# Kernel tuning notes

Hardware: AMD Instinct MI355X
Metric: run time of the kernel (lower is better)

The kernel has to match this reference:

```python
import jax, jax.numpy as jnp
import numpy as np

B, T, C, H = 8, 1024, 1024, 16
D = C // H
EPS = 1e-5

def _ln(x, g, b):
    mu = jnp.mean(x, axis=-1, keepdims=True)
    var = jnp.var(x, axis=-1, keepdims=True)
    return (x - mu) * jax.lax.rsqrt(var + EPS) * g + b

def _build_mask(cond_mask, cond_len, token_len):
    # Vectorized form of the per-batch Python-loop mask in the torch module.
    counts = jnp.sum(cond_mask, axis=-1)            # [B] number of valid cond tokens
    rows = jnp.arange(T)
    cols = jnp.arange(T)
    # all rows may attend to the first counts[i] (cond) columns
    m_cond = cols[None, None, :] < counts[:, None, None]          # [B,1,T]
    m_cond = jnp.broadcast_to(m_cond, (B, T, T))
    # block-causal tiled pattern on rows/cols >= cond_len:
    # value = (col - cond_len) % token_len <= (row - cond_len) % token_len
    pattern = ((cols[None, :] - cond_len) % token_len) <= ((rows[:, None] - cond_len) % token_len)
    m_block = (rows[:, None] >= cond_len) & (cols[None, :] >= cond_len) & pattern  # [T,T]
    # cols >= cond_len: overwritten by block pattern (rows < cond_len stay 0 there)
    mask = jnp.where(cols[None, None, :] < cond_len, m_cond, m_block[None, :, :])
    return mask[:, None, :, :]                      # [B,1,T,T] bool

def _attn(x, Wq, bq, Wk, bk, Wv, bv, Wp, bp, cond_mask, cond_len, token_len):
    q = (x @ Wq + bq).reshape(B, T, H, D).transpose(0, 2, 1, 3)  # [B,H,T,D]
    k = (x @ Wk + bk).reshape(B, T, H, D).transpose(0, 2, 1, 3)
    v = (x @ Wv + bv).reshape(B, T, H, D).transpose(0, 2, 1, 3)
    att = jnp.einsum('bhqd,bhkd->bhqk', q, k) * (1.0 / np.sqrt(D))
    mask = _build_mask(cond_mask, cond_len, token_len)
    att = jnp.where(mask, att, -jnp.inf)
    att = jax.nn.softmax(att, axis=-1)
    y = jnp.einsum('bhqk,bhkd->bhqd', att, v)
    y = y.transpose(0, 2, 1, 3).reshape(B, T, C)
    return y @ Wp + bp

def setup_inputs() -> dict:
    key = jax.random.key(0)
    ks = jax.random.split(key, 16)
    cond_len, token_len = 256, 768
    s = 1.0 / np.sqrt(C)
    counts = jax.random.randint(ks[0], (B,), 1, cond_len + 1)
    cond_mask = (jnp.arange(T)[None, :] < counts[:, None]).astype(jnp.int32)
    return {
        'x': jax.random.normal(ks[1], (B, T, C), jnp.float32),
        'ln1_g': jnp.ones((C,), jnp.float32), 'ln1_b': jnp.zeros((C,), jnp.float32),
        'Wq': jax.random.normal(ks[2], (C, C), jnp.float32) * s, 'bq': jnp.zeros((C,), jnp.float32),
        'Wk': jax.random.normal(ks[3], (C, C), jnp.float32) * s, 'bk': jnp.zeros((C,), jnp.float32),
        'Wv': jax.random.normal(ks[4], (C, C), jnp.float32) * s, 'bv': jnp.zeros((C,), jnp.float32),
        'Wp': jax.random.normal(ks[5], (C, C), jnp.float32) * s, 'bp': jnp.zeros((C,), jnp.float32),
        'ln2_g': jnp.ones((C,), jnp.float32), 'ln2_b': jnp.zeros((C,), jnp.float32),
        'W1': jax.random.normal(ks[6], (C, 4 * C), jnp.float32) * s, 'b1': jnp.zeros((4 * C,), jnp.float32),
        'W2': jax.random.normal(ks[7], (4 * C, C), jnp.float32) * (0.5 * s), 'b2': jnp.zeros((C,), jnp.float32),
        'cond_mask': cond_mask,
        'cond_len': cond_len,
        'token_len': token_len,
    }

def reference(x, ln1_g, ln1_b, Wq, bq, Wk, bk, Wv, bv, Wp, bp, ln2_g, ln2_b, W1, b1, W2, b2, cond_mask, cond_len, token_len):
    x = x + _attn(_ln(x, ln1_g, ln1_b), Wq, bq, Wk, bk, Wv, bv, Wp, bp, cond_mask, cond_len, token_len)
    h = _ln(x, ln2_g, ln2_b)
    x = x + (jax.nn.gelu(h @ W1 + b1, approximate=False) @ W2 + b2)
    return x
```

## Files before the change

kernel.cpp:

```cpp
#include <hip/hip_runtime.h>
#include <hip/hip_bf16.h>
#include <cstdint>
#include <cstddef>

typedef __attribute__((ext_vector_type(8))) short short8;
typedef __attribute__((ext_vector_type(4))) float f32x4;
typedef __attribute__((ext_vector_type(4))) unsigned short us4;

#define MFMA_BF16(a, b, c) __builtin_amdgcn_mfma_f32_16x16x32_bf16((a), (b), (c), 0, 0, 0)
#define VMCNT(n) asm volatile("s_waitcnt vmcnt(" #n ")" ::: "memory")

__device__ __forceinline__ unsigned short f2bf(float f) {
  unsigned int u = __float_as_uint(f);
  u += 0x7FFFu + ((u >> 16) & 1u);
  return (unsigned short)(u >> 16);
}

typedef const void __attribute__((address_space(1)))* as1_cvp;
typedef void __attribute__((address_space(3)))* as3_vp;
__device__ __forceinline__ void gll16(const short* g, short* l) {
#if defined(__HIP_DEVICE_COMPILE__)
  __builtin_amdgcn_global_load_lds((as1_cvp)g, (as3_vp)l, 16, 0, 0);
#else
  (void)g; (void)l;
#endif
}

__global__ void count_kernel(const int* __restrict__ cm, int* __restrict__ counts) {
  __shared__ int sd[256];
  const int b = blockIdx.x, t = threadIdx.x;
  int s = 0;
  for (int i = t; i < 1024; i += 256) s += cm[b * 1024 + i];
  sd[t] = s; __syncthreads();
  for (int k = 128; k > 0; k >>= 1) { if (t < k) sd[t] += sd[t + k]; __syncthreads(); }
  if (t == 0) counts[b] = sd[0];
}

__global__ void pack_bias_kernel(const float* __restrict__ bq, const float* __restrict__ bk,
                                 const float* __restrict__ bv, float* __restrict__ dst) {
  int i = blockIdx.x * 256 + threadIdx.x;
  dst[i] = (i < 1024) ? bq[i] : (i < 2048 ? bk[i - 1024] : bv[i - 2048]);
}

__global__ void transpose_kernel(const float* __restrict__ src, unsigned short* __restrict__ dst,
                                 int R, int C) {
  __shared__ float tile[32][33];
  const int c0 = blockIdx.x * 32, r0 = blockIdx.y * 32;
  const int tx = threadIdx.x, ty = threadIdx.y;
  #pragma unroll
  for (int i = ty; i < 32; i += 8)
    tile[i][tx] = src[(size_t)(r0 + i) * C + (c0 + tx)];
  __syncthreads();
  #pragma unroll
  for (int i = ty; i < 32; i += 8)
    dst[(size_t)(c0 + i) * R + (r0 + tx)] = f2bf(tile[tx][i]);
}

__global__ void vtrans_kernel(const short* __restrict__ qkv, short* __restrict__ vtr) {
  __shared__ short tile[32][33];
  const int bh = blockIdx.z;
  const int t0 = blockIdx.x * 32, d0 = blockIdx.y * 32;
  const int b = bh >> 4, h = bh & 15;
  const int tx = threadIdx.x, ty = threadIdx.y;
  const short* src = qkv + (size_t)b * 1024 * 3072 + 2048 + h * 64;
  #pragma unroll
  for (int i = ty; i < 32; i += 8)
    tile[i][tx] = src[(size_t)(t0 + i) * 3072 + d0 + tx];
  __syncthreads();
  short* dst = vtr + (size_t)bh * 65536;
  #pragma unroll
  for (int i = ty; i < 32; i += 8)
    dst[(d0 + i) * 1024 + t0 + tx] = tile[tx][i];
}

__global__ __launch_bounds__(256) void ln_kernel(const float* __restrict__ in,
                                                 const float* __restrict__ gw,
                                                 const float* __restrict__ bw,
                                                 unsigned short* __restrict__ out) {
  const int row = blockIdx.x, t = threadIdx.x;
  const float4 v = ((const float4*)(in + (size_t)row * 1024))[t];
  float s = v.x + v.y + v.z + v.w;
  float ss = v.x * v.x + v.y * v.y + v.z * v.z + v.w * v.w;
  #pragma unroll
  for (int o = 32; o >= 1; o >>= 1) { s += __shfl_down(s, o, 64); ss += __shfl_down(ss, o, 64); }
  __shared__ float red[8];
  if ((t & 63) == 0) { red[t >> 6] = s; red[4 + (t >> 6)] = ss; }
  __syncthreads();
  const float S  = red[0] + red[1] + red[2] + red[3];
  const float SS = red[4] + red[5] + red[6] + red[7];
  const float mu = S * (1.0f / 1024.0f);
  const float var = SS * (1.0f / 1024.0f) - mu * mu;
  const float rs = rsqrtf(var + 1e-5f);
  const int c = t * 4;
  const float4 g4 = ((const float4*)gw)[t];
  const float4 b4 = ((const float4*)bw)[t];
  us4 o4;
  o4[0] = f2bf((v.x - mu) * rs * g4.x + b4.x);
  o4[1] = f2bf((v.y - mu) * rs * g4.y + b4.y);
  o4[2] = f2bf((v.z - mu) * rs * g4.z + b4.z);
  o4[3] = f2bf((v.w - mu) * rs * g4.w + b4.w);
  *(us4*)(out + (size_t)row * 1024 + c) = o4;
}

template <int EPI>
__global__ __launch_bounds__(512, 1) void gemm_k2_kernel(
    const short* __restrict__ A, const short* __restrict__ BT,
    const float* __restrict__ bias, int N, int K, int gm,
    unsigned short* __restrict__ outb, float* __restrict__ outf,
    const float* __restrict__ res) {
  __shared__ alignas(16) short lds[73728];
  const int t = threadIdx.x;
  const int l = t & 63, w = t >> 6;
  const int lq = l & 15, g = l >> 4;
  const int wr = w >> 2, wc = w & 3;
  const int cpx = (int)gridDim.x >> 3;
  const int wid = ((int)blockIdx.x & 7) * cpx + ((int)blockIdx.x >> 3);
  const int bm = (wid % gm) * 256, bn = (wid / gm) * 128;
  const int NT = K >> 6;

  const int csw = ((t & 7) ^ ((t >> 3) & 7)) * 8;
  const int sA = t >> 3;
  const int sB = ((t >> 8) & 1) * 64 + ((t >> 3) & 31);

  const f32x4 z4 = {0.f, 0.f, 0.f, 0.f};
  f32x4 acc[8][2];
  #pragma unroll
  for (int i = 0; i < 8; i++) { acc[i][0] = z4; acc[i][1] = z4; }

  auto stageA = [&](int buf, int h, int k0) {
    const short* src = A + (size_t)(bm + h * 64 + sA) * K + k0 + csw;
    short* dst = lds + buf * 24576 + h * 8192 + t * 8;
    gll16(src, dst);
    gll16(src + (size_t)128 * K, dst + 4096);
  };
  auto stageB = [&](int buf, int h, int k0) {
    const short* src = BT + (size_t)(bn + h * 32 + sB) * K + k0 + csw;
    short* dst = lds + buf * 24576 + 16384 + h * 4096 + t * 8;
    gll16(src, dst);
  };
  auto rdA = [&](int buf, int mh, int mi2, int kk) {
    const int ra = wr * 64 + mi2 * 16 + lq;
    const int unit = (kk * 4 + g) ^ (ra & 7);
    return *(const short8*)(lds + buf * 24576 + mh * 8192 + ra * 64 + unit * 8);
  };
  auto rdB = [&](int buf, int ni2, int kk) {
    const int h = wc & 1;
    const int rb = (wc >> 1) * 32 + ni2 * 16 + lq;
    const int unit = (kk * 4 + g) ^ (rb & 7);
    return *(const short8*)(lds + buf * 24576 + 16384 + h * 4096 + rb * 64 + unit * 8);
  };

  stageA(0, 0, 0);  stageB(0, 0, 0);
  stageA(0, 1, 0);  stageB(0, 1, 0);
  stageA(1, 0, 64); stageB(1, 0, 64);
  VMCNT(3);
  __builtin_amdgcn_s_barrier();

  int cur = 0;
  for (int v = 0; v < NT; ++v) {
    const int nx1 = (cur == 2) ? 0 : cur + 1;
    const int nx2 = (nx1 == 2) ? 0 : nx1 + 1;
    short8 a[4][2], b[2][2], a2[4][2];
    #pragma unroll
    for (int mi2 = 0; mi2 < 4; ++mi2)
      #pragma unroll
      for (int kk = 0; kk < 2; ++kk) a[mi2][kk] = rdA(cur, 0, mi2, kk);
    #pragma unroll
    for (int ni2 = 0; ni2 < 2; ++ni2)
      #pragma unroll
      for (int kk = 0; kk < 2; ++kk) b[ni2][kk] = rdB(cur, ni2, kk);
    if (v + 1 < NT) { stageA(nx1, 1, (v + 1) * 64); stageB(nx1, 1, (v + 1) * 64); }
    __builtin_amdgcn_s_setprio(1);
    #pragma unroll
    for (int mi2 = 0; mi2 < 4; ++mi2)
      #pragma unroll
      for (int ni2 = 0; ni2 < 2; ++ni2)
        #pragma unroll
        for (int kk = 0; kk < 2; ++kk)
          acc[mi2][ni2] = MFMA_BF16(a[mi2][kk], b[ni2][kk], acc[mi2][ni2]);
    __builtin_amdgcn_s_setprio(0);
    #pragma unroll
    for (int mi2 = 0; mi2 < 4; ++mi2)
      #pragma unroll
      for (int kk = 0; kk < 2; ++kk) a2[mi2][kk] = rdA(cur, 1, mi2, kk);
    if (v + 2 < NT) {
      stageA(nx2, 0, (v + 2) * 64); stageB(nx2, 0, (v + 2) * 64);
      VMCNT(3);
    } else {
      VMCNT(0);
    }
    __builtin_amdgcn_s_barrier();
    __builtin_amdgcn_s_setprio(1);
    #pragma unroll
    for (int mi2 = 0; mi2 < 4; ++mi2)
      #pragma unroll
      for (int ni2 = 0; ni2 < 2; ++ni2)
        #pragma unroll
        for (int kk = 0; kk < 2; ++kk)
          acc[4 + mi2][ni2] = MFMA_BF16(a2[mi2][kk], b[ni2][kk], acc[4 + mi2][ni2]);
    __builtin_amdgcn_s_setprio(0);
    cur = nx1;
  }

  if (EPI == 2) {
    #pragma unroll
    for (int mi = 0; mi < 8; ++mi) {
      #pragma unroll
      for (int ni = 0; ni < 2; ++ni) {
        const int col = bn + wc * 32 + ni * 16 + lq;
        const float bv = bias[col];
        #pragma unroll
        for (int r = 0; r < 4; ++r) {
          const int row = bm + wr * 128 + (mi >> 2) * 64 + (mi & 3) * 16 + 4 * g + r;
          const size_t idx = (size_t)row * N + col;
          outf[idx] = acc[mi][ni][r] + bv + res[idx];
        }
      }
    }
    return;
  }

  unsigned short* eb = (unsigned short*)lds;
  #pragma unroll
  for (int mi = 0; mi < 8; ++mi) {
    #pragma unroll
    for (int ni = 0; ni < 2; ++ni) {
      const int col = wc * 32 + ni * 16 + lq;
      const float bv = bias[bn + col];
      #pragma unroll
      for (int r = 0; r < 4; ++r) {
        const int row = wr * 128 + (mi >> 2) * 64 + (mi & 3) * 16 + 4 * g + r;
        float vv = acc[mi][ni][r] + bv;
        if (EPI == 1) vv = 0.5f * vv * (1.0f + erff(vv * 0.70710678118654752440f));
        eb[row * 128 + col] = f2bf(vv);
      }
    }
  }
  __syncthreads();
  #pragma unroll
  for (int it = 0; it < 8; ++it) {
    const int unit = it * 512 + t;
    const int row = unit >> 4, c8 = unit & 15;
    const short8 vv = *(const short8*)(lds + unit * 8);
    *(short8*)((short*)outb + (size_t)(bm + row) * N + bn + c8 * 8) = vv;
  }
}

__global__ __launch_bounds__(64) void attn_kernel(
    const short* __restrict__ qkv, const short* __restrict__ vtr,
    unsigned short* __restrict__ y, const int* __restrict__ counts) {
  const int blk = blockIdx.x;
  const int slot = blk >> 3;
  const int p = slot & 31;
  const int bh = ((slot >> 5) << 3) | (blk & 7);
  const int b = bh >> 4, h = bh & 15;
  const int l = threadIdx.x & 63;
  const int lq = l & 15, g = l >> 4;
  const int qb0 = p * 16, qb1 = (63 - p) * 16;
  const int count = counts[b];

  const short* base  = qkv + (size_t)b * 1024 * 3072 + h * 64;
  const short* vbase = vtr + (size_t)bh * 65536;

  short8 qf[2][2];
  {
    const short* qr0 = base + (size_t)(qb0 + lq) * 3072 + 8 * g;
    const short* qr1 = base + (size_t)(qb1 + lq) * 3072 + 8 * g;
    qf[0][0] = *(const short8*)qr0; qf[0][1] = *(const short8*)(qr0 + 32);
    qf[1][0] = *(const short8*)qr1; qf[1][1] = *(const short8*)(qr1 + 32);
  }

  const f32x4 z4 = {0.f, 0.f, 0.f, 0.f};
  f32x4 oacc[2][4];
  #pragma unroll
  for (int grp = 0; grp < 2; ++grp)
    #pragma unroll
    for (int dc = 0; dc < 4; ++dc) oacc[grp][dc] = z4;
  float mrun[2] = {-1e30f, -1e30f};
  float lrun[2] = {0.f, 0.f};
  const int permrow = 8 * (lq >> 2) + (lq & 3);
  const float SC = 0.125f * 1.44269504088896f;

  const int ncond = min((count + 31) >> 5, 8);
  const int ncausal = (qb1 + 16 - 256 + 31) >> 5;
  const int nt = ncond + ncausal;
  auto kv_of = [&](int i) { return i < ncond ? i * 32 : 256 + (i - ncond) * 32; };

  auto loadt = [&](int kv0, short8 (&kr)[4], short8 (&vr)[4]) {
    const short* ka = base + (size_t)(kv0 + permrow) * 3072 + 1024 + 8 * g;
    kr[0] = *(const short8*)ka;
    kr[1] = *(const short8*)(ka + 32);
    kr[2] = *(const short8*)(ka + 4 * 3072);
    kr[3] = *(const short8*)(ka + 4 * 3072 + 32);
    #pragma unroll
    for (int dc = 0; dc < 4; ++dc)
      vr[dc] = *(const short8*)(vbase + (16 * dc + lq) * 1024 + kv0 + 8 * g);
  };

  auto compute = [&](int i, const short8 (&kr)[4], const short8 (&vr)[4]) {
    const int kv0 = kv_of(i);
    const bool isCond = (i < ncond);
    #pragma unroll
    for (int grp = 0; grp < 2; ++grp) {
      const int qb = grp ? qb1 : qb0;
      if (!isCond && kv0 >= qb + 16) continue;
      const bool needMask = isCond ? (kv0 + 32 > count) : (kv0 + 31 > qb);
      f32x4 sA = z4, sB = z4;
      __builtin_amdgcn_s_setprio(1);
      sA = MFMA_BF16(kr[0], qf[grp][0], sA);
      sA = MFMA_BF16(kr[1], qf[grp][1], sA);
      sB = MFMA_BF16(kr[2], qf[grp][0], sB);
      sB = MFMA_BF16(kr[3], qf[grp][1], sB);
      __builtin_amdgcn_s_setprio(0);
      const int q = qb + lq;
      float mx = -1e30f;
      if (needMask) {
        #pragma unroll
        for (int r = 0; r < 4; ++r) {
          const int colA = kv0 + 8 * g + r, colB = colA + 4;
          const bool okA = isCond ? (colA < count) : (colA <= q);
          const bool okB = isCond ? (colB < count) : (colB <= q);
          const float vA = okA ? sA[r] * SC : -1e30f;
          const float vB = okB ? sB[r] * SC : -1e30f;
          sA[r] = vA; sB[r] = vB;
          mx = fmaxf(fmaxf(vA, vB), mx);
        }
      } else {
        #pragma unroll
        for (int r = 0; r < 4; ++r) {
          const float vA = sA[r] * SC, vB = sB[r] * SC;
          sA[r] = vA; sB[r] = vB;
          mx = fmaxf(fmaxf(vA, vB), mx);
        }
      }
      mx = fmaxf(mx, __shfl_xor(mx, 16, 64));
      mx = fmaxf(mx, __shfl_xor(mx, 32, 64));
      float m = mrun[grp];
      if (!__all(mx <= m + 8.0f)) {
        const float mn = fmaxf(m, mx);
        const float sf = exp2f(m - mn);
        lrun[grp] *= sf;
        #pragma unroll
        for (int dc = 0; dc < 4; ++dc)
          #pragma unroll
          for (int r = 0; r < 4; ++r) oacc[grp][dc][r] *= sf;
        mrun[grp] = mn; m = mn;
      }
      float ps = 0.f;
      #pragma unroll
      for (int r = 0; r < 4; ++r) {
        const float aa = exp2f(sA[r] - m);
        const float c2 = exp2f(sB[r] - m);
        sA[r] = aa; sB[r] = c2; ps += aa + c2;
      }
      ps += __shfl_xor(ps, 16, 64);
      ps += __shfl_xor(ps, 32, 64);
      lrun[grp] += ps;
      union { short8 s8; __hip_bfloat162 h2[4]; } pu;
      pu.h2[0] = __float22bfloat162_rn(float2{sA[0], sA[1]});
      pu.h2[1] = __float22bfloat162_rn(float2{sA[2], sA[3]});
      pu.h2[2] = __float22bfloat162_rn(float2{sB[0], sB[1]});
      pu.h2[3] = __float22bfloat162_rn(float2{sB[2], sB[3]});
      __builtin_amdgcn_s_setprio(1);
      #pragma unroll
      for (int dc = 0; dc < 4; ++dc)
        oacc[grp][dc] = MFMA_BF16(vr[dc], pu.s8, oacc[grp][dc]);
      __builtin_amdgcn_s_setprio(0);
    }
  };

  short8 kb0[4], vb0[4], kb1[4], vb1[4];
  loadt(kv_of(0), kb0, vb0);
  for (int i = 0; i < nt; i += 2) {
    if (i + 1 < nt) loadt(kv_of(i + 1), kb1, vb1);
    compute(i, kb0, vb0);
    if (i + 1 >= nt) break;
    if (i + 2 < nt) loadt(kv_of(i + 2), kb0, vb0);
    compute(i + 1, kb1, vb1);
  }

  #pragma unroll
  for (int grp = 0; grp < 2; ++grp) {
    const int qb = grp ? qb1 : qb0;
    const float inv = 1.0f / lrun[grp];
    unsigned short* yr = y + (size_t)(b * 1024 + qb + lq) * 1024 + h * 64;
    #pragma unroll
    for (int dc = 0; dc < 4; ++dc)
      #pragma unroll
      for (int r = 0; r < 4; ++r)
        yr[16 * dc + 4 * g + r] = f2bf(oacc[grp][dc][r] * inv);
  }
}

extern "C" void kernel_launch(void* const* d_in, const int* in_sizes, int n_in,
                              void* d_out, int out_size, void* d_ws, size_t ws_size,
                              hipStream_t stream) {
  (void)in_sizes; (void)n_in; (void)out_size; (void)ws_size;
  const float* x     = (const float*)d_in[0];
  const float* ln1_g = (const float*)d_in[1];
  const float* ln1_b = (const float*)d_in[2];
  const float* Wq    = (const float*)d_in[3];
  const float* bq    = (const float*)d_in[4];
  const float* Wk    = (const float*)d_in[5];
  const float* bk    = (const float*)d_in[6];
  const float* Wv    = (const float*)d_in[7];
  const float* bv    = (const float*)d_in[8];
  const float* Wp    = (const float*)d_in[9];
  const float* bp    = (const float*)d_in[10];
  const float* ln2_g = (const float*)d_in[11];
  const float* ln2_b = (const float*)d_in[12];
  const float* W1    = (const float*)d_in[13];
  const float* b1    = (const float*)d_in[14];
  const float* W2    = (const float*)d_in[15];
  const float* b2    = (const float*)d_in[16];
  const int* cond_mask = (const int*)d_in[17];

  char* ws = (char*)d_ws;
  const size_t MB = 1u << 20;
  short* xn    = (short*)(ws + 0);
  short* vtr   = (short*)(ws + 0);
  short* qkv   = (short*)(ws + 16 * MB);
  short* act   = (short*)(ws + 0);
  unsigned short* yb = (unsigned short*)(ws + 64 * MB);
  float* x1    = (float*)(ws + 80 * MB);
  short* hb    = (short*)(ws + 112 * MB);
  short* wqkvT = (short*)(ws + 128 * MB);
  short* wpT   = (short*)(ws + 134 * MB);
  short* w1T   = (short*)(ws + 136 * MB);
  short* w2T   = (short*)(ws + 144 * MB);
  float* bqkv  = (float*)(ws + 152 * MB);
  int* counts  = (int*)(ws + 152 * MB + 16384);

  const dim3 tb(32, 8);
  count_kernel<<<8, 256, 0, stream>>>(cond_mask, counts);
  pack_bias_kernel<<<12, 256, 0, stream>>>(bq, bk, bv, bqkv);
  transpose_kernel<<<dim3(32, 32), tb, 0, stream>>>(Wq, (unsigned short*)wqkvT, 1024, 1024);
  transpose_kernel<<<dim3(32, 32), tb, 0, stream>>>(Wk, (unsigned short*)(wqkvT + 1024 * 1024), 1024, 1024);
  transpose_kernel<<<dim3(32, 32), tb, 0, stream>>>(Wv, (unsigned short*)(wqkvT + 2 * 1024 * 1024), 1024, 1024);
  transpose_kernel<<<dim3(32, 32), tb, 0, stream>>>(Wp, (unsigned short*)wpT, 1024, 1024);
  transpose_kernel<<<dim3(128, 32), tb, 0, stream>>>(W1, (unsigned short*)w1T, 1024, 4096);
  transpose_kernel<<<dim3(32, 128), tb, 0, stream>>>(W2, (unsigned short*)w2T, 4096, 1024);
  ln_kernel<<<8192, 256, 0, stream>>>(x, ln1_g, ln1_b, (unsigned short*)xn);

  gemm_k2_kernel<0><<<768, 512, 0, stream>>>(xn, wqkvT, bqkv, 3072, 1024, 32,
                                             (unsigned short*)qkv, nullptr, nullptr);
  vtrans_kernel<<<dim3(32, 2, 128), tb, 0, stream>>>(qkv, vtr);
  attn_kernel<<<4096, 64, 0, stream>>>(qkv, vtr, yb, counts);
  gemm_k2_kernel<2><<<256, 512, 0, stream>>>((const short*)yb, wpT, bp, 1024, 1024, 32,
                                             nullptr, x1, x);
  ln_kernel<<<8192, 256, 0, stream>>>(x1, ln2_g, ln2_b, (unsigned short*)hb);
  gemm_k2_kernel<1><<<1024, 512, 0, stream>>>(hb, w1T, b1, 4096, 1024, 32,
                                              (unsigned short*)act, nullptr, nullptr);
  gemm_k2_kernel<2><<<256, 512, 0, stream>>>(act, w2T, b2, 1024, 4096, 32,
                                             nullptr, (float*)d_out, x1);
}
```

Baseline: 471.5 us.

## Add 128x256 GEMM tile kernel for QKV and MLP-up projections

```diff
diff --git a/kernel.cpp b/kernel.cpp
--- a/kernel.cpp
+++ b/kernel.cpp
@@ -103,11 +103,137 @@
 }
 
 template <int EPI>
+__global__ __launch_bounds__(512, 1) void gemm_n256_kernel(
+    const short* __restrict__ A, const short* __restrict__ BT,
+    const float* __restrict__ bias, int N, int K, int gm,
+    unsigned short* __restrict__ outb) {
+  __shared__ alignas(16) short lds[73728];
+  const int t = threadIdx.x;
+  const int l = t & 63, w = t >> 6;
+  const int lq = l & 15, g = l >> 4;
+  const int wr = w >> 2, wc = w & 3;
+  const int cpx = (int)gridDim.x >> 3;
+  const int wid = ((int)blockIdx.x & 7) * cpx + ((int)blockIdx.x >> 3);
+  const int bm = (wid % gm) * 128, bn = (wid / gm) * 256;
+  const int NT = K >> 6;
+
+  const int csw = ((t & 7) ^ ((t >> 3) & 7)) * 8;
+  const int sr = t >> 3;
+
+  const f32x4 z4 = {0.f, 0.f, 0.f, 0.f};
+  f32x4 acc[4][4];
+  #pragma unroll
+  for (int i = 0; i < 4; i++)
+    #pragma unroll
+    for (int j = 0; j < 4; j++) acc[i][j] = z4;
+
+  auto stageA = [&](int buf, int k0) {
+    const short* src = A + (size_t)(bm + sr) * K + k0 + csw;
+    short* dst = lds + buf * 24576 + t * 8;
+    gll16(src, dst);
+    gll16(src + (size_t)64 * K, dst + 4096);
+  };
+  auto stageB = [&](int buf, int h, int k0) {
+    const short* src = BT + (size_t)(bn + h * 128 + sr) * K + k0 + csw;
+    short* dst = lds + buf * 24576 + 8192 + h * 8192 + t * 8;
+    gll16(src, dst);
+    gll16(src + (size_t)64 * K, dst + 4096);
+  };
+  auto rdA = [&](int buf, int mi2, int kk) {
+    const int ra = wr * 64 + mi2 * 16 + lq;
+    const int unit = (kk * 4 + g) ^ (ra & 7);
+    return *(const short8*)(lds + buf * 24576 + ra * 64 + unit * 8);
+  };
+  auto rdB = [&](int buf, int h, int ni2, int kk) {
+    const int cb = wc * 32 + ni2 * 16 + lq;
+    const int unit = (kk * 4 + g) ^ (cb & 7);
+    return *(const short8*)(lds + buf * 24576 + 8192 + h * 8192 + cb * 64 + unit * 8);
+  };
+
+  stageA(0, 0);     stageB(0, 0, 0);
+  stageB(0, 1, 0);
+  stageA(1, 64);    stageB(1, 0, 64);
+  VMCNT(4);
+  __builtin_amdgcn_s_barrier();
+
+  int cur = 0;
+  for (int v = 0; v < NT; ++v) {
+    const int nx1 = (cur == 2) ? 0 : cur + 1;
+    const int nx2 = (nx1 == 2) ? 0 : nx1 + 1;
+    short8 a[4][2], b[2][2], b2[2][2];
+    #pragma unroll
+    for (int mi2 = 0; mi2 < 4; ++mi2)
+      #pragma unroll
+      for (int kk = 0; kk < 2; ++kk) a[mi2][kk] = rdA(cur, mi2, kk);
+    #pragma unroll
+    for (int ni2 = 0; ni2 < 2; ++ni2)
+      #pragma unroll
+      for (int kk = 0; kk < 2; ++kk) b[ni2][kk] = rdB(cur, 0, ni2, kk);
+    if (v + 1 < NT) stageB(nx1, 1, (v + 1) * 64);
+    __builtin_amdgcn_s_setprio(1);
+    #pragma unroll
+    for (int mi2 = 0; mi2 < 4; ++mi2)
+      #pragma unroll
+      for (int ni2 = 0; ni2 < 2; ++ni2)
+        #pragma unroll
+        for (int kk = 0; kk < 2; ++kk)
+          acc[mi2][ni2] = MFMA_BF16(a[mi2][kk], b[ni2][kk], acc[mi2][ni2]);
+    __builtin_amdgcn_s_setprio(0);
+    #pragma unroll
+    for (int ni2 = 0; ni2 < 2; ++ni2)
+      #pragma unroll
+      for (int kk = 0; kk < 2; ++kk) b2[ni2][kk] = rdB(cur, 1, ni2, kk);
+    if (v + 2 < NT) {
+      stageA(nx2, (v + 2) * 64); stageB(nx2, 0, (v + 2) * 64);
+      VMCNT(4);
+    } else {
+      VMCNT(0);
+    }
+    __builtin_amdgcn_s_barrier();
+    __builtin_amdgcn_s_setprio(1);
+    #pragma unroll
+    for (int mi2 = 0; mi2 < 4; ++mi2)
+      #pragma unroll
+      for (int ni2 = 0; ni2 < 2; ++ni2)
+        #pragma unroll
+        for (int kk = 0; kk < 2; ++kk)
+          acc[mi2][2 + ni2] = MFMA_BF16(a[mi2][kk], b2[ni2][kk], acc[mi2][2 + ni2]);
+    __builtin_amdgcn_s_setprio(0);
+    cur = nx1;
+  }
+
+  __syncthreads();
+  unsigned short* eb = (unsigned short*)lds;
+  #pragma unroll
+  for (int mi2 = 0; mi2 < 4; ++mi2) {
+    #pragma unroll
+    for (int n = 0; n < 4; ++n) {
+      const int col = (n >> 1) * 128 + wc * 32 + (n & 1) * 16 + lq;
+      const float bv = bias[bn + col];
+      #pragma unroll
+      for (int r = 0; r < 4; ++r) {
+        const int row = wr * 64 + mi2 * 16 + 4 * g + r;
+        float vv = acc[mi2][n][r] + bv;
+        if (EPI == 1) vv = 0.5f * vv * (1.0f + erff(vv * 0.70710678118654752440f));
+        eb[row * 256 + col] = f2bf(vv);
+      }
+    }
+  }
+  __syncthreads();
+  #pragma unroll
+  for (int it = 0; it < 8; ++it) {
+    const int unit = it * 512 + t;
+    const int row = unit >> 5, c8 = unit & 31;
+    const short8 vv = *(const short8*)(lds + unit * 8);
+    *(short8*)((short*)outb + (size_t)(bm + row) * N + bn + c8 * 8) = vv;
+  }
+}
+
+template <int EPI>
 __global__ __launch_bounds__(512, 1) void gemm_k2_kernel(
     const short* __restrict__ A, const short* __restrict__ BT,
     const float* __restrict__ bias, int N, int K, int gm,
-    unsigned short* __restrict__ outb, float* __restrict__ outf,
-    const float* __restrict__ res) {
+    float* __restrict__ outf, const float* __restrict__ res) {
   __shared__ alignas(16) short lds[73728];
   const int t = threadIdx.x;
   const int l = t & 63, w = t >> 6;
@@ -202,47 +328,19 @@
     cur = nx1;
   }
 
-  if (EPI == 2) {
-    #pragma unroll
-    for (int mi = 0; mi < 8; ++mi) {
-      #pragma unroll
-      for (int ni = 0; ni < 2; ++ni) {
-        const int col = bn + wc * 32 + ni * 16 + lq;
-        const float bv = bias[col];
-        #pragma unroll
-        for (int r = 0; r < 4; ++r) {
-          const int row = bm + wr * 128 + (mi >> 2) * 64 + (mi & 3) * 16 + 4 * g + r;
-          const size_t idx = (size_t)row * N + col;
-          outf[idx] = acc[mi][ni][r] + bv + res[idx];
-        }
+  #pragma unroll
+  for (int mi = 0; mi < 8; ++mi) {
+    #pragma unroll
+    for (int ni = 0; ni < 2; ++ni) {
+      const int col = bn + wc * 32 + ni * 16 + lq;
+      const float bv = bias[col];
+      #pragma unroll
+      for (int r = 0; r < 4; ++r) {
+        const int row = bm + wr * 128 + (mi >> 2) * 64 + (mi & 3) * 16 + 4 * g + r;
+        const size_t idx = (size_t)row * N + col;
+        outf[idx] = acc[mi][ni][r] + bv + res[idx];
       }
     }
-    return;
-  }
-
-  unsigned short* eb = (unsigned short*)lds;
-  #pragma unroll
-  for (int mi = 0; mi < 8; ++mi) {
-    #pragma unroll
-    for (int ni = 0; ni < 2; ++ni) {
-      const int col = wc * 32 + ni * 16 + lq;
-      const float bv = bias[bn + col];
-      #pragma unroll
-      for (int r = 0; r < 4; ++r) {
-        const int row = wr * 128 + (mi >> 2) * 64 + (mi & 3) * 16 + 4 * g + r;
-        float vv = acc[mi][ni][r] + bv;
-        if (EPI == 1) vv = 0.5f * vv * (1.0f + erff(vv * 0.70710678118654752440f));
-        eb[row * 128 + col] = f2bf(vv);
-      }
-    }
-  }
-  __syncthreads();
-  #pragma unroll
-  for (int it = 0; it < 8; ++it) {
-    const int unit = it * 512 + t;
-    const int row = unit >> 4, c8 = unit & 15;
-    const short8 vv = *(const short8*)(lds + unit * 8);
-    *(short8*)((short*)outb + (size_t)(bm + row) * N + bn + c8 * 8) = vv;
   }
 }
 
@@ -442,15 +540,15 @@
   transpose_kernel<<<dim3(32, 128), tb, 0, stream>>>(W2, (unsigned short*)w2T, 4096, 1024);
   ln_kernel<<<8192, 256, 0, stream>>>(x, ln1_g, ln1_b, (unsigned short*)xn);
 
-  gemm_k2_kernel<0><<<768, 512, 0, stream>>>(xn, wqkvT, bqkv, 3072, 1024, 32,
-                                             (unsigned short*)qkv, nullptr, nullptr);
+  gemm_n256_kernel<0><<<768, 512, 0, stream>>>(xn, wqkvT, bqkv, 3072, 1024, 64,
+                                               (unsigned short*)qkv);
   vtrans_kernel<<<dim3(32, 2, 128), tb, 0, stream>>>(qkv, vtr);
   attn_kernel<<<4096, 64, 0, stream>>>(qkv, vtr, yb, counts);
   gemm_k2_kernel<2><<<256, 512, 0, stream>>>((const short*)yb, wpT, bp, 1024, 1024, 32,
-                                             nullptr, x1, x);
+                                             x1, x);
   ln_kernel<<<8192, 256, 0, stream>>>(x1, ln2_g, ln2_b, (unsigned short*)hb);
-  gemm_k2_kernel<1><<<1024, 512, 0, stream>>>(hb, w1T, b1, 4096, 1024, 32,
-                                              (unsigned short*)act, nullptr, nullptr);
+  gemm_n256_kernel<1><<<1024, 512, 0, stream>>>(hb, w1T, b1, 4096, 1024, 64,
+                                                (unsigned short*)act);
   gemm_k2_kernel<2><<<256, 512, 0, stream>>>(act, w2T, b2, 1024, 4096, 32,
-                                             nullptr, (float*)d_out, x1);
-}
+                                             (float*)d_out, x1);
+}
```

Measured after the change: 462.3 us. Within noise of the previous version (-1.9%).
